# Performance work log

Measured on AMD Instinct MI355X. Metric: run time of the kernel, lower is better.

The kernel has to match this reference:

```python
import jax, jax.numpy as jnp
import numpy as np

N_NODES = 100000
N_EDGES = 1600000
FEAT = 128
EMBED = 128
N_CLASSES = 40
N_BATCH = 1024


def setup_inputs() -> dict:
    key = jax.random.key(0)
    ks = jax.random.split(key, 8)
    features = jax.random.normal(ks[0], (N_NODES, FEAT), dtype=jnp.float32)
    edge_src = jax.random.randint(ks[1], (N_EDGES,), 0, N_NODES, dtype=jnp.int32)
    edge_dst = jnp.sort(jax.random.randint(ks[2], (N_EDGES,), 0, N_NODES, dtype=jnp.int32))
    batch_nodes = jax.random.randint(ks[3], (N_BATCH,), 0, N_NODES, dtype=jnp.int32)
    s1 = 1.0 / np.sqrt(FEAT)
    s2 = 1.0 / np.sqrt(EMBED)
    W1 = jax.random.normal(ks[4], (FEAT, EMBED), dtype=jnp.float32) * s1
    b1 = jnp.zeros((EMBED,), dtype=jnp.float32)
    W2 = jax.random.normal(ks[5], (EMBED, EMBED), dtype=jnp.float32) * s2
    b2 = jnp.zeros((EMBED,), dtype=jnp.float32)
    Wl = jax.random.normal(ks[6], (EMBED, N_CLASSES), dtype=jnp.float32) * s2
    bl = jnp.zeros((N_CLASSES,), dtype=jnp.float32)
    return dict(features=features, edge_src=edge_src, edge_dst=edge_dst,
                batch_nodes=batch_nodes, W1=W1, b1=b1, W2=W2, b2=b2, Wl=Wl, bl=bl)


def _sage_conv(x, edge_src, edge_dst, W, b):
    # GraphSAGE-mean: mean over {self} U neighbors, then linear + ReLU.
    msg = jnp.take(x, edge_src, axis=0)                      # [E, d] gather
    agg = jax.ops.segment_sum(msg, edge_dst, num_segments=N_NODES)
    deg = jax.ops.segment_sum(jnp.ones((edge_src.shape[0],), x.dtype),
                              edge_dst, num_segments=N_NODES)
    mean = (agg + x) / (deg + 1.0)[:, None]                  # include self-loop
    return jax.nn.relu(mean @ W + b)


def reference(features, edge_src, edge_dst, batch_nodes, W1, b1, W2, b2, Wl, bl):
    x = _sage_conv(features, edge_src, edge_dst, W1, b1)      # conv1: [N, EMBED]
    x = _sage_conv(x, edge_src, edge_dst, W2, b2)             # conv2: [N, EMBED]
    x = jnp.take(x, batch_nodes, axis=0)                      # restrict to batch
    logits = x @ Wl + bl                                       # [B, C]
    return jax.nn.log_softmax(logits, axis=1)
```

## Files before the change

kernel.cpp:

```cpp
#include <hip/hip_runtime.h>
#include <hip/hip_bf16.h>
#include <math.h>

#define N_NODES 100000
#define N_EDGES 1600000
#define FEAT 128
#define EMBED 128
#define N_CLASSES 40
#define N_BATCH 1024

#define RPB 4
#define NTHREADS 512
#define LCAP 512
#define CHUNK 128
#define APAD 132

__global__ __launch_bounds__(256) void offsets_kernel(
    const int* __restrict__ dst, int* __restrict__ off) {
  int i = blockIdx.x * 256 + threadIdx.x;
  if (i >= N_EDGES) return;
  int d1 = dst[i];
  int d0 = (i == 0) ? -1 : dst[i - 1];
  for (int d = d0 + 1; d <= d1; ++d) off[d] = i;
  if (i == N_EDGES - 1) {
    for (int d = d1 + 1; d <= N_NODES; ++d) off[d] = N_EDGES;
  }
}

__device__ __forceinline__ float2 gather_mean(
    const float2* __restrict__ x2, const int* __restrict__ esrc,
    int e0, int e1, int lane, float2 self) {
  const int deg = e1 - e0;
  float ax0 = self.x, ay0 = self.y;
  float ax1 = 0.f, ay1 = 0.f;
  float ax2 = 0.f, ay2 = 0.f;
  float ax3 = 0.f, ay3 = 0.f;
  while (e0 < e1) {
    int cnt = e1 - e0;
    if (cnt > 64) cnt = 64;
    int s = (lane < cnt) ? esrc[e0 + lane] : 0;
    int j = 0;
    for (; j + 8 <= cnt; j += 8) {
      int s0 = __shfl(s, j + 0), s1 = __shfl(s, j + 1);
      int s2 = __shfl(s, j + 2), s3 = __shfl(s, j + 3);
      int s4 = __shfl(s, j + 4), s5 = __shfl(s, j + 5);
      int s6 = __shfl(s, j + 6), s7 = __shfl(s, j + 7);
      float2 v0 = x2[(size_t)s0 * 64 + lane];
      float2 v1 = x2[(size_t)s1 * 64 + lane];
      float2 v2 = x2[(size_t)s2 * 64 + lane];
      float2 v3 = x2[(size_t)s3 * 64 + lane];
      float2 v4 = x2[(size_t)s4 * 64 + lane];
      float2 v5 = x2[(size_t)s5 * 64 + lane];
      float2 v6 = x2[(size_t)s6 * 64 + lane];
      float2 v7 = x2[(size_t)s7 * 64 + lane];
      ax0 += v0.x; ay0 += v0.y;
      ax1 += v1.x; ay1 += v1.y;
      ax2 += v2.x; ay2 += v2.y;
      ax3 += v3.x; ay3 += v3.y;
      ax0 += v4.x; ay0 += v4.y;
      ax1 += v5.x; ay1 += v5.y;
      ax2 += v6.x; ay2 += v6.y;
      ax3 += v7.x; ay3 += v7.y;
    }
    for (; j < cnt; ++j) {
      int sj = __shfl(s, j);
      float2 v = x2[(size_t)sj * 64 + lane];
      ax0 += v.x; ay0 += v.y;
    }
    e0 += cnt;
  }
  const float inv = 1.0f / (float)(deg + 1);
  float2 o;
  o.x = (ax0 + ax1 + ax2 + ax3) * inv;
  o.y = (ay0 + ay1 + ay2 + ay3) * inv;
  return o;
}

__global__ __launch_bounds__(NTHREADS) void mega_kernel(
    const float* __restrict__ x, const int* __restrict__ esrc,
    const int* __restrict__ off, const int* __restrict__ batch,
    const float* __restrict__ W1, const float* __restrict__ b1,
    const float* __restrict__ W2, const float* __restrict__ b2,
    const float* __restrict__ Wl, const float* __restrict__ bl,
    float* __restrict__ out) {
  __shared__ float meanA[CHUNK][APAD];
  __shared__ float acc2[RPB][128];
  __shared__ int list[LCAP];
  __shared__ int segs[RPB], sege[RPB], nodes[RPB], degs[RPB], e0s[RPB];
  __shared__ int Lsh;

  const int tid = threadIdx.x;
  const int lane = tid & 63;
  const int wv = tid >> 6;

  if (tid < RPB) {
    int node = batch[blockIdx.x * RPB + tid];
    nodes[tid] = node;
    int e0 = off[node], e1 = off[node + 1];
    e0s[tid] = e0;
    degs[tid] = e1 - e0;
  }
  __syncthreads();
  if (tid == 0) {
    int pos = 0;
    for (int r = 0; r < RPB; ++r) {
      segs[r] = pos;
      int d = degs[r];
      if (pos + d + 1 > LCAP) d = LCAP - pos - 1;
      pos += d + 1;
      sege[r] = pos;
    }
    Lsh = pos;
  }
  __syncthreads();
  for (int r = 0; r < RPB; ++r) {
    int s0 = segs[r], d = sege[r] - s0 - 1, e0 = e0s[r];
    for (int j = tid; j < d; j += NTHREADS) list[s0 + j] = esrc[e0 + j];
    if (tid == 0) list[sege[r] - 1] = nodes[r];
  }
  for (int i = tid; i < RPB * 128; i += NTHREADS) ((float*)acc2)[i] = 0.f;
  __syncthreads();

  const int L = Lsh;
  const float2* __restrict__ x2 = (const float2*)x;
  float* __restrict__ flat = &meanA[0][0];

  for (int c0 = 0; c0 < L; c0 += CHUNK) {
    const int clen = min(CHUNK, L - c0);

    for (int sc = wv; sc < clen; sc += 8) {
      int node = list[c0 + sc];
      int e0 = off[node], e1 = off[node + 1];
      float2 self = x2[(size_t)node * 64 + lane];
      float2 o = gather_mean(x2, esrc, e0, e1, lane, self);
      meanA[2 * lane][sc] = o.x;
      meanA[2 * lane + 1][sc] = o.y;
    }
    __syncthreads();

    const int ty = tid >> 4;
    const int tx = tid & 15;
    float accg[4][8];
#pragma unroll
    for (int i = 0; i < 4; ++i)
#pragma unroll
      for (int j = 0; j < 8; ++j) accg[i][j] = 0.f;
#pragma unroll 4
    for (int k = 0; k < 128; ++k) {
      float4 a = *(const float4*)&meanA[k][ty * 4];
      float4 bq0 = *(const float4*)&W1[(size_t)k * 128 + tx * 8];
      float4 bq1 = *(const float4*)&W1[(size_t)k * 128 + tx * 8 + 4];
      float av[4] = {a.x, a.y, a.z, a.w};
      float bv[8] = {bq0.x, bq0.y, bq0.z, bq0.w, bq1.x, bq1.y, bq1.z, bq1.w};
#pragma unroll
      for (int i = 0; i < 4; ++i)
#pragma unroll
        for (int j = 0; j < 8; ++j) accg[i][j] = fmaf(av[i], bv[j], accg[i][j]);
    }
    __syncthreads();

    {
      float bb[8];
#pragma unroll
      for (int j = 0; j < 8; ++j) bb[j] = b1[tx * 8 + j];
#pragma unroll
      for (int i = 0; i < 4; ++i) {
        int s = ty * 4 + i;
        if (s < clen) {
          float4 o0, o1;
          o0.x = fmaxf(accg[i][0] + bb[0], 0.f);
          o0.y = fmaxf(accg[i][1] + bb[1], 0.f);
          o0.z = fmaxf(accg[i][2] + bb[2], 0.f);
          o0.w = fmaxf(accg[i][3] + bb[3], 0.f);
          o1.x = fmaxf(accg[i][4] + bb[4], 0.f);
          o1.y = fmaxf(accg[i][5] + bb[5], 0.f);
          o1.z = fmaxf(accg[i][6] + bb[6], 0.f);
          o1.w = fmaxf(accg[i][7] + bb[7], 0.f);
          *(float4*)&flat[s * APAD + tx * 8] = o0;
          *(float4*)&flat[s * APAD + tx * 8 + 4] = o1;
        }
      }
    }
    __syncthreads();

    {
      int r = wv & 3;
      int col = ((wv >> 2) << 6) | lane;
      int s0 = max(segs[r] - c0, 0);
      int s1 = min(sege[r] - c0, clen);
      float a = 0.f;
      for (int s = s0; s < s1; ++s) a += flat[s * APAD + col];
      acc2[r][col] += a;
    }
    __syncthreads();
  }

  if (tid < RPB * 128) {
    int r = tid >> 7;
    acc2[r][tid & 127] *= 1.0f / (float)(degs[r] + 1);
  }
  float* Wls = flat;
  float* h2s = flat + 128 * N_CLASSES;
  for (int i = tid; i < (128 * N_CLASSES) / 4; i += NTHREADS)
    ((float4*)Wls)[i] = ((const float4*)Wl)[i];
  __syncthreads();

  {
    const int r = tid >> 7;
    const int c = tid & 127;
    float acc = 0.f;
#pragma unroll 4
    for (int k = 0; k < 128; ++k)
      acc = fmaf(acc2[r][k], W2[(size_t)k * 128 + c], acc);
    h2s[r * 128 + c] = fmaxf(acc + b2[c], 0.f);
  }
  __syncthreads();

  if (wv < RPB) {
    const int r = wv;
    float s = -3.0e38f;
    if (lane < N_CLASSES) {
      s = bl[lane];
      for (int k = 0; k < 128; ++k)
        s = fmaf(h2s[r * 128 + k], Wls[k * N_CLASSES + lane], s);
    }
    float m = s;
#pragma unroll
    for (int o = 32; o > 0; o >>= 1) m = fmaxf(m, __shfl_xor(m, o));
    float e = (lane < N_CLASSES) ? expf(s - m) : 0.f;
    float tot = e;
#pragma unroll
    for (int o = 32; o > 0; o >>= 1) tot += __shfl_xor(tot, o);
    if (lane < N_CLASSES)
      out[(size_t)(blockIdx.x * RPB + r) * N_CLASSES + lane] = s - m - logf(tot);
  }
}

extern "C" void kernel_launch(void* const* d_in, const int* in_sizes, int n_in,
                              void* d_out, int out_size, void* d_ws, size_t ws_size,
                              hipStream_t stream) {
  const float* features = (const float*)d_in[0];
  const int* edge_src   = (const int*)d_in[1];
  const int* edge_dst   = (const int*)d_in[2];
  const int* batch      = (const int*)d_in[3];
  const float* W1       = (const float*)d_in[4];
  const float* b1       = (const float*)d_in[5];
  const float* W2       = (const float*)d_in[6];
  const float* b2       = (const float*)d_in[7];
  const float* Wl       = (const float*)d_in[8];
  const float* bl       = (const float*)d_in[9];
  float* out = (float*)d_out;

  int* off = (int*)d_ws;

  offsets_kernel<<<(N_EDGES + 255) / 256, 256, 0, stream>>>(edge_dst, off);
  mega_kernel<<<N_BATCH / RPB, NTHREADS, 0, stream>>>(
      features, edge_src, off, batch, W1, b1, W2, b2, Wl, bl, out);
}
```

Before: 163.2 us.

## Process one batch node per block to spread gathers across more CUs

The fused kernel now handles a single batch node per block instead of four, launching 1024 blocks rather than 256. This is meant to fill more compute units and hide the latency of the irregular two-hop gathers. The first-layer transform now computes one row per 16-thread group, with W1 read from global memory and no register tiling across rows. The neighbor list is capped at 63 per node, and launch bounds request higher occupancy. In exchange, the layer-1 GEMM loses its register reuse, and the W2 and Wl weights are re-read by four times as many blocks.

```diff
diff --git a/kernel.cpp b/kernel.cpp
--- a/kernel.cpp
+++ b/kernel.cpp
@@ -9,10 +9,8 @@
 #define N_CLASSES 40
 #define N_BATCH 1024
 
-#define RPB 4
 #define NTHREADS 512
-#define LCAP 512
-#define CHUNK 128
+#define SCAP 64
 #define APAD 132
 
 __global__ __launch_bounds__(256) void offsets_kernel(
@@ -76,153 +74,118 @@
   return o;
 }
 
-__global__ __launch_bounds__(NTHREADS) void mega_kernel(
+__global__ __launch_bounds__(NTHREADS, 8) void mega_kernel(
     const float* __restrict__ x, const int* __restrict__ esrc,
     const int* __restrict__ off, const int* __restrict__ batch,
     const float* __restrict__ W1, const float* __restrict__ b1,
     const float* __restrict__ W2, const float* __restrict__ b2,
     const float* __restrict__ Wl, const float* __restrict__ bl,
     float* __restrict__ out) {
-  __shared__ float meanA[CHUNK][APAD];
-  __shared__ float acc2[RPB][128];
-  __shared__ int list[LCAP];
-  __shared__ int segs[RPB], sege[RPB], nodes[RPB], degs[RPB], e0s[RPB];
-  __shared__ int Lsh;
+  __shared__ float sA[SCAP][APAD];
+  __shared__ float red[EMBED];
+  __shared__ float h2s[EMBED];
+  __shared__ int list[SCAP];
+  __shared__ int info[3];
 
   const int tid = threadIdx.x;
   const int lane = tid & 63;
   const int wv = tid >> 6;
 
-  if (tid < RPB) {
-    int node = batch[blockIdx.x * RPB + tid];
-    nodes[tid] = node;
-    int e0 = off[node], e1 = off[node + 1];
-    e0s[tid] = e0;
-    degs[tid] = e1 - e0;
-  }
-  __syncthreads();
   if (tid == 0) {
-    int pos = 0;
-    for (int r = 0; r < RPB; ++r) {
-      segs[r] = pos;
-      int d = degs[r];
-      if (pos + d + 1 > LCAP) d = LCAP - pos - 1;
-      pos += d + 1;
-      sege[r] = pos;
-    }
-    Lsh = pos;
-  }
-  __syncthreads();
-  for (int r = 0; r < RPB; ++r) {
-    int s0 = segs[r], d = sege[r] - s0 - 1, e0 = e0s[r];
-    for (int j = tid; j < d; j += NTHREADS) list[s0 + j] = esrc[e0 + j];
-    if (tid == 0) list[sege[r] - 1] = nodes[r];
-  }
-  for (int i = tid; i < RPB * 128; i += NTHREADS) ((float*)acc2)[i] = 0.f;
-  __syncthreads();
-
-  const int L = Lsh;
+    int node = batch[blockIdx.x];
+    int e0 = off[node];
+    int e1 = off[node + 1];
+    info[0] = e0;
+    info[1] = e1 - e0;
+    info[2] = node;
+  }
+  __syncthreads();
+  const int e0b = info[0];
+  const int degb = info[1];
+  const int nodeb = info[2];
+  const int dclamp = (degb > SCAP - 1) ? (SCAP - 1) : degb;
+  const int L = dclamp + 1;
+
+  for (int j = tid; j < dclamp; j += NTHREADS) list[j] = esrc[e0b + j];
+  if (tid == 0) list[dclamp] = nodeb;
+  __syncthreads();
+
   const float2* __restrict__ x2 = (const float2*)x;
-  float* __restrict__ flat = &meanA[0][0];
-
-  for (int c0 = 0; c0 < L; c0 += CHUNK) {
-    const int clen = min(CHUNK, L - c0);
-
-    for (int sc = wv; sc < clen; sc += 8) {
-      int node = list[c0 + sc];
-      int e0 = off[node], e1 = off[node + 1];
-      float2 self = x2[(size_t)node * 64 + lane];
-      float2 o = gather_mean(x2, esrc, e0, e1, lane, self);
-      meanA[2 * lane][sc] = o.x;
-      meanA[2 * lane + 1][sc] = o.y;
+  for (int sc = wv; sc < L; sc += 8) {
+    int n = list[sc];
+    int a0 = off[n], a1 = off[n + 1];
+    float2 self = x2[(size_t)n * 64 + lane];
+    float2 o = gather_mean(x2, esrc, a0, a1, lane, self);
+    *(float2*)&sA[sc][2 * lane] = o;
+  }
+  __syncthreads();
+
+  const int ty = tid >> 4;
+  const int tx = tid & 15;
+  float bb[8];
+#pragma unroll
+  for (int j = 0; j < 8; ++j) bb[j] = b1[tx * 8 + j];
+
+  for (int s0 = 0; s0 < L; s0 += 32) {
+    const int s = s0 + ty;
+    float accg[8];
+#pragma unroll
+    for (int j = 0; j < 8; ++j) accg[j] = 0.f;
+    if (s < L) {
+#pragma unroll 4
+      for (int k = 0; k < 128; ++k) {
+        float a = sA[s][k];
+        float4 bq0 = *(const float4*)&W1[(size_t)k * 128 + tx * 8];
+        float4 bq1 = *(const float4*)&W1[(size_t)k * 128 + tx * 8 + 4];
+        accg[0] = fmaf(a, bq0.x, accg[0]);
+        accg[1] = fmaf(a, bq0.y, accg[1]);
+        accg[2] = fmaf(a, bq0.z, accg[2]);
+        accg[3] = fmaf(a, bq0.w, accg[3]);
+        accg[4] = fmaf(a, bq1.x, accg[4]);
+        accg[5] = fmaf(a, bq1.y, accg[5]);
+        accg[6] = fmaf(a, bq1.z, accg[6]);
+        accg[7] = fmaf(a, bq1.w, accg[7]);
+      }
     }
     __syncthreads();
-
-    const int ty = tid >> 4;
-    const int tx = tid & 15;
-    float accg[4][8];
-#pragma unroll
-    for (int i = 0; i < 4; ++i)
-#pragma unroll
-      for (int j = 0; j < 8; ++j) accg[i][j] = 0.f;
-#pragma unroll 4
-    for (int k = 0; k < 128; ++k) {
-      float4 a = *(const float4*)&meanA[k][ty * 4];
-      float4 bq0 = *(const float4*)&W1[(size_t)k * 128 + tx * 8];
-      float4 bq1 = *(const float4*)&W1[(size_t)k * 128 + tx * 8 + 4];
-      float av[4] = {a.x, a.y, a.z, a.w};
-      float bv[8] = {bq0.x, bq0.y, bq0.z, bq0.w, bq1.x, bq1.y, bq1.z, bq1.w};
-#pragma unroll
-      for (int i = 0; i < 4; ++i)
-#pragma unroll
-        for (int j = 0; j < 8; ++j) accg[i][j] = fmaf(av[i], bv[j], accg[i][j]);
+    if (s < L) {
+      float4 o0, o1;
+      o0.x = fmaxf(accg[0] + bb[0], 0.f);
+      o0.y = fmaxf(accg[1] + bb[1], 0.f);
+      o0.z = fmaxf(accg[2] + bb[2], 0.f);
+      o0.w = fmaxf(accg[3] + bb[3], 0.f);
+      o1.x = fmaxf(accg[4] + bb[4], 0.f);
+      o1.y = fmaxf(accg[5] + bb[5], 0.f);
+      o1.z = fmaxf(accg[6] + bb[6], 0.f);
+      o1.w = fmaxf(accg[7] + bb[7], 0.f);
+      *(float4*)&sA[s][tx * 8] = o0;
+      *(float4*)&sA[s][tx * 8 + 4] = o1;
     }
     __syncthreads();
-
-    {
-      float bb[8];
-#pragma unroll
-      for (int j = 0; j < 8; ++j) bb[j] = b1[tx * 8 + j];
-#pragma unroll
-      for (int i = 0; i < 4; ++i) {
-        int s = ty * 4 + i;
-        if (s < clen) {
-          float4 o0, o1;
-          o0.x = fmaxf(accg[i][0] + bb[0], 0.f);
-          o0.y = fmaxf(accg[i][1] + bb[1], 0.f);
-          o0.z = fmaxf(accg[i][2] + bb[2], 0.f);
-          o0.w = fmaxf(accg[i][3] + bb[3], 0.f);
-          o1.x = fmaxf(accg[i][4] + bb[4], 0.f);
-          o1.y = fmaxf(accg[i][5] + bb[5], 0.f);
-          o1.z = fmaxf(accg[i][6] + bb[6], 0.f);
-          o1.w = fmaxf(accg[i][7] + bb[7], 0.f);
-          *(float4*)&flat[s * APAD + tx * 8] = o0;
-          *(float4*)&flat[s * APAD + tx * 8 + 4] = o1;
-        }
-      }
-    }
-    __syncthreads();
-
-    {
-      int r = wv & 3;
-      int col = ((wv >> 2) << 6) | lane;
-      int s0 = max(segs[r] - c0, 0);
-      int s1 = min(sege[r] - c0, clen);
-      float a = 0.f;
-      for (int s = s0; s < s1; ++s) a += flat[s * APAD + col];
-      acc2[r][col] += a;
-    }
-    __syncthreads();
-  }
-
-  if (tid < RPB * 128) {
-    int r = tid >> 7;
-    acc2[r][tid & 127] *= 1.0f / (float)(degs[r] + 1);
-  }
-  float* Wls = flat;
-  float* h2s = flat + 128 * N_CLASSES;
-  for (int i = tid; i < (128 * N_CLASSES) / 4; i += NTHREADS)
-    ((float4*)Wls)[i] = ((const float4*)Wl)[i];
-  __syncthreads();
-
-  {
-    const int r = tid >> 7;
-    const int c = tid & 127;
-    float acc = 0.f;
+  }
+
+  if (tid < 128) {
+    float ssum = 0.f;
+    for (int s = 0; s < L; ++s) ssum += sA[s][tid];
+    red[tid] = ssum * (1.0f / (float)(degb + 1));
+  }
+  __syncthreads();
+
+  if (tid < 128) {
+    float a = 0.f;
 #pragma unroll 4
     for (int k = 0; k < 128; ++k)
-      acc = fmaf(acc2[r][k], W2[(size_t)k * 128 + c], acc);
-    h2s[r * 128 + c] = fmaxf(acc + b2[c], 0.f);
-  }
-  __syncthreads();
-
-  if (wv < RPB) {
-    const int r = wv;
+      a = fmaf(red[k], W2[(size_t)k * 128 + tid], a);
+    h2s[tid] = fmaxf(a + b2[tid], 0.f);
+  }
+  __syncthreads();
+
+  if (wv == 0) {
     float s = -3.0e38f;
     if (lane < N_CLASSES) {
       s = bl[lane];
       for (int k = 0; k < 128; ++k)
-        s = fmaf(h2s[r * 128 + k], Wls[k * N_CLASSES + lane], s);
+        s = fmaf(h2s[k], Wl[k * N_CLASSES + lane], s);
     }
     float m = s;
 #pragma unroll
@@ -232,7 +195,7 @@
 #pragma unroll
     for (int o = 32; o > 0; o >>= 1) tot += __shfl_xor(tot, o);
     if (lane < N_CLASSES)
-      out[(size_t)(blockIdx.x * RPB + r) * N_CLASSES + lane] = s - m - logf(tot);
+      out[(size_t)blockIdx.x * N_CLASSES + lane] = s - m - logf(tot);
   }
 }
 
@@ -254,6 +217,6 @@
   int* off = (int*)d_ws;
 
   offsets_kernel<<<(N_EDGES + 255) / 256, 256, 0, stream>>>(edge_dst, off);
-  mega_kernel<<<N_BATCH / RPB, NTHREADS, 0, stream>>>(
+  mega_kernel<<<N_BATCH, NTHREADS, 0, stream>>>(
       features, edge_src, off, batch, W1, b1, W2, b2, Wl, bl, out);
 }
```

Result: slower. 187.8 us (+15.1%).
